# Performance work log

Hardware: AMD Instinct MI355X
Metric: run time of the kernel (lower is better)

Reference implementation:

```python
import jax, jax.numpy as jnp
import numpy as np
from jax import lax

EPS = 1e-5
DW_TH = 4.0   # threshold in cut_conv3_5_DW
PW_TH = 1e-3  # threshold in cut_conv3_5_PW


def _bn(x, gamma, beta, mean, var):
    # inference-mode batchnorm over channel dim (NCHW)
    scale = (gamma * lax.rsqrt(var + EPS))[None, :, None, None]
    shift = (beta - mean * gamma * lax.rsqrt(var + EPS))[None, :, None, None]
    return x * scale + shift


def _channel_cut(x, th):
    # faithful to max(torch.max(x[m][k]), -torch.min(x[m][k])) == max |x| per (n, c)
    max_obs = jnp.max(jnp.abs(x), axis=(2, 3), keepdims=True)  # [N, C, 1, 1]
    return jnp.where(max_obs < th, jnp.zeros_like(x), x)


def setup_inputs() -> dict:
    key = jax.random.key(0)
    ks = jax.random.split(key, 6)
    N, Cin, Cout, H, W = 32, 256, 512, 56, 56
    x = jax.random.normal(ks[0], (N, Cin, H, W), dtype=jnp.float32)
    dw_w = jax.random.normal(ks[1], (Cin, 1, 3, 3), dtype=jnp.float32) * 0.3
    dw_b = jax.random.normal(ks[2], (Cin,), dtype=jnp.float32) * 0.1
    pw_w = jax.random.normal(ks[3], (Cout, Cin), dtype=jnp.float32) * 0.05
    pw_b = jax.random.normal(ks[4], (Cout,), dtype=jnp.float32) * 0.1
    return {
        "x": x,
        "dw_w": dw_w,
        "dw_b": dw_b,
        "bn1_gamma": jnp.ones((Cin,), jnp.float32) * 2.0,
        "bn1_beta": jnp.zeros((Cin,), jnp.float32),
        "bn1_mean": jnp.zeros((Cin,), jnp.float32),
        "bn1_var": jnp.ones((Cin,), jnp.float32),
        "pw_w": pw_w,
        "pw_b": pw_b,
        "bn2_gamma": jnp.ones((Cout,), jnp.float32),
        "bn2_beta": jnp.zeros((Cout,), jnp.float32),
        "bn2_mean": jnp.zeros((Cout,), jnp.float32),
        "bn2_var": jnp.ones((Cout,), jnp.float32),
    }


def reference(x, dw_w, dw_b, bn1_gamma, bn1_beta, bn1_mean, bn1_var,
              pw_w, pw_b, bn2_gamma, bn2_beta, bn2_mean, bn2_var):
    Cin = x.shape[1]
    # depthwise 3x3 conv, padding=1 (groups == in_channels)
    y = lax.conv_general_dilated(
        x, dw_w, window_strides=(1, 1), padding=((1, 1), (1, 1)),
        dimension_numbers=("NCHW", "OIHW", "NCHW"),
        feature_group_count=Cin,
    ) + dw_b[None, :, None, None]
    y = jax.nn.relu(_bn(y, bn1_gamma, bn1_beta, bn1_mean, bn1_var))
    y = _channel_cut(y, DW_TH)
    # pointwise 1x1 conv as channel GEMM
    z = jnp.einsum("oc,nchw->nohw", pw_w, y) + pw_b[None, :, None, None]
    z = jax.nn.relu(_bn(z, bn2_gamma, bn2_beta, bn2_mean, bn2_var))
    z = _channel_cut(z, PW_TH)
    return z
```

## Files before the change

kernel.cpp:

```cpp
#include <hip/hip_runtime.h>
#include <hip/hip_bf16.h>

#define HH 56
#define WW 56
#define HW 3136
#define CIN 256
#define COUT 512
#define NBATCH 32
#define EPS 1e-5f
#define DW_TH 4.0f
#define PW_TH 1e-3f

#define CG 32
#define CPITCH 508

typedef __attribute__((ext_vector_type(8))) short s16x8;
typedef __attribute__((ext_vector_type(4))) float f32x4;
typedef unsigned int u32;
typedef unsigned short u16;

__device__ __forceinline__ void async_copy16(void* lds, const void* g) {
    __builtin_amdgcn_global_load_lds((const __attribute__((address_space(1))) unsigned int*)g,
                                     (__attribute__((address_space(3))) unsigned int*)lds,
                                     16, 0, 0);
}

__device__ __forceinline__ u16 bf16_bits(float f) {
    __hip_bfloat16 h = __float2bfloat16(f);
    union { __hip_bfloat16 h; u16 u; } cv; cv.h = h; return cv.u;
}

__global__ __launch_bounds__(256) void prep_kernel(
    const float* __restrict__ pww, const float* __restrict__ pwb,
    const float* __restrict__ g2, const float* __restrict__ b2,
    const float* __restrict__ m2, const float* __restrict__ v2,
    u16* __restrict__ wb, float2* __restrict__ scsh,
    u32* __restrict__ omax, u32* __restrict__ dwmax)
{
    const int gid = blockIdx.x * 256 + threadIdx.x;
    const int base = gid * 8;
    const float4 a = *(const float4*)(pww + base);
    const float4 b = *(const float4*)(pww + base + 4);
    union { u16 u[8]; s16x8 v; } pk;
    pk.u[0] = bf16_bits(a.x); pk.u[1] = bf16_bits(a.y);
    pk.u[2] = bf16_bits(a.z); pk.u[3] = bf16_bits(a.w);
    pk.u[4] = bf16_bits(b.x); pk.u[5] = bf16_bits(b.y);
    pk.u[6] = bf16_bits(b.z); pk.u[7] = bf16_bits(b.w);
    *(s16x8*)(wb + base) = pk.v;
    omax[gid] = 0u;
    if (gid < NBATCH * CIN) dwmax[gid] = 0u;
    if (gid < COUT) {
        const float sc = g2[gid] * rsqrtf(v2[gid] + EPS);
        const float sh = fmaf(-m2[gid], sc, b2[gid]) + pwb[gid] * sc;
        scsh[gid] = make_float2(sc, sh);
    }
}

__global__ __launch_bounds__(256) void dw_kernel(
    const float* __restrict__ x, const float* __restrict__ dww, const float* __restrict__ dwb,
    const float* __restrict__ g1, const float* __restrict__ b1,
    const float* __restrict__ m1, const float* __restrict__ v1,
    u16* __restrict__ y, u32* __restrict__ dwmax)
{
    __shared__ float xs[CG * CPITCH];

    const int bid = blockIdx.x;
    const int cg = bid & 7;
    const int hs = (bid >> 3) & 7;
    const int n  = bid >> 6;
    const int t  = threadIdx.x;

    const int g0     = hs * 7 - 1;
    const int gstart = (g0 < 0) ? 0 : g0;
    const int gend   = (hs * 7 + 7 > 55) ? 55 : hs * 7 + 7;
    const int nrows  = gend - gstart + 1;
    const int dst0   = gstart - g0;
    const int cnt4   = nrows * 14;

    if (hs == 0) {
        for (int i = t; i < CG * 14; i += 256) {
            const int c = i / 14, j = i - c * 14;
            *(float4*)&xs[c * CPITCH + j * 4] = make_float4(0.f, 0.f, 0.f, 0.f);
        }
    } else if (hs == 7) {
        for (int i = t; i < CG * 14; i += 256) {
            const int c = i / 14, j = i - c * 14;
            *(float4*)&xs[c * CPITCH + 8 * 56 + j * 4] = make_float4(0.f, 0.f, 0.f, 0.f);
        }
    }

    {
        const float* gbase = x + (size_t)(n * CIN + cg * CG) * HW + gstart * 56;
        const int half = t >> 7;
        const int i4 = t & 127;
        for (int cc = 0; cc < 16; ++cc) {
            const int c = cc * 2 + half;
            if (i4 < cnt4) {
                const float4 v = *(const float4*)(gbase + (size_t)c * HW + i4 * 4);
                *(float4*)&xs[c * CPITCH + dst0 * 56 + i4 * 4] = v;
            }
        }
    }
    __syncthreads();

    const int r = t >> 5;
    const int c = t & 31;
    float vmax = 0.f;
    if (r < 7) {
        const int ch = cg * CG + c;
        const float* wp = dww + ch * 9;
        const float w00 = wp[0], w01 = wp[1], w02 = wp[2];
        const float w10 = wp[3], w11 = wp[4], w12 = wp[5];
        const float w20 = wp[6], w21 = wp[7], w22 = wp[8];
        const float sc = g1[ch] * rsqrtf(v1[ch] + EPS);
        const float sh = fmaf(-m1[ch], sc, b1[ch]) + dwb[ch] * sc;

        const float* rm = &xs[c * CPITCH + r * 56];
        const float* r0 = rm + 56;
        const float* rp = rm + 112;
        const int grow = hs * 7 + r;
        u16* yo = y + (size_t)(n * HW + grow * WW) * CIN + ch;

        float4 cm = *(const float4*)rm;
        float4 c0 = *(const float4*)r0;
        float4 cp = *(const float4*)rp;
        float lm = 0.f, l0 = 0.f, lp = 0.f;

        for (int chk = 0; chk < 14; ++chk) {
            float4 nm, n0, np;
            if (chk < 13) {
                nm = *(const float4*)(rm + 4 * chk + 4);
                n0 = *(const float4*)(r0 + 4 * chk + 4);
                np = *(const float4*)(rp + 4 * chk + 4);
            } else {
                nm = n0 = np = make_float4(0.f, 0.f, 0.f, 0.f);
            }
            float s0 = w00*lm   + w01*cm.x + w02*cm.y
                     + w10*l0   + w11*c0.x + w12*c0.y
                     + w20*lp   + w21*cp.x + w22*cp.y;
            float s1 = w00*cm.x + w01*cm.y + w02*cm.z
                     + w10*c0.x + w11*c0.y + w12*c0.z
                     + w20*cp.x + w21*cp.y + w22*cp.z;
            float s2 = w00*cm.y + w01*cm.z + w02*cm.w
                     + w10*c0.y + w11*c0.z + w12*c0.w
                     + w20*cp.y + w21*cp.z + w22*cp.w;
            float s3 = w00*cm.z + w01*cm.w + w02*nm.x
                     + w10*c0.z + w11*c0.w + w12*n0.x
                     + w20*cp.z + w21*cp.w + w22*np.x;
            const float v0 = fmaxf(fmaf(s0, sc, sh), 0.f);
            const float v1s = fmaxf(fmaf(s1, sc, sh), 0.f);
            const float v2s = fmaxf(fmaf(s2, sc, sh), 0.f);
            const float v3 = fmaxf(fmaf(s3, sc, sh), 0.f);
            vmax = fmaxf(fmaxf(vmax, fmaxf(v0, v1s)), fmaxf(v2s, v3));
            yo[(4 * chk + 0) * CIN] = bf16_bits(v0);
            yo[(4 * chk + 1) * CIN] = bf16_bits(v1s);
            yo[(4 * chk + 2) * CIN] = bf16_bits(v2s);
            yo[(4 * chk + 3) * CIN] = bf16_bits(v3);
            lm = cm.w; l0 = c0.w; lp = cp.w;
            cm = nm; c0 = n0; cp = np;
        }
    }
    vmax = fmaxf(vmax, __shfl_xor(vmax, 32));
    if ((t & 32) == 0)
        atomicMax(&dwmax[n * CIN + cg * CG + c], __float_as_uint(vmax));
}

__global__ __launch_bounds__(64) void dwcut_kernel(const u32* __restrict__ dwmax, u16* __restrict__ y)
{
    const int b = blockIdx.x;
    if (__uint_as_float(dwmax[b]) >= DW_TH) return;
    const int n = b >> 8, c = b & 255;
    for (int hw = threadIdx.x; hw < HW; hw += 64)
        y[(size_t)(n * HW + hw) * CIN + c] = 0;
}

__global__ __launch_bounds__(256) void pw_kernel(
    const u16* __restrict__ y, const u16* __restrict__ wb,
    const float2* __restrict__ scsh,
    float* __restrict__ out, u32* __restrict__ omax)
{
    __shared__ u16 Wt[128 * 32];
    __shared__ u16 Yt[112 * 32];

    const int hwt = blockIdx.x, ot = blockIdx.y, n = blockIdx.z;
    const int t = threadIdx.x;
    const int w = t >> 6;
    const int l = t & 63;
    const int lo = l & 15, hi = l >> 4;

    const int o_blk  = ot * 128;
    const int hw_blk = n * HW + hwt * 112;

    const u16* wg  = wb + (size_t)(o_blk + w * 32 + (l >> 2)) * CIN + (l & 3) * 8;
    const u16* yg  = y  + (size_t)(hw_blk + (l >> 2)) * CIN + (l & 3) * 8;
    char* WtB = (char*)Wt;
    char* YtB = (char*)Yt;

    f32x4 acc[2][7];
#pragma unroll
    for (int s = 0; s < 2; ++s)
#pragma unroll
        for (int j = 0; j < 7; ++j) acc[s][j] = (f32x4){0.f, 0.f, 0.f, 0.f};

    for (int k0 = 0; k0 < CIN; k0 += 32) {
        async_copy16(WtB + (w * 32 + 0) * 64, wg + k0);
        async_copy16(WtB + (w * 32 + 16) * 64, wg + k0 + (size_t)16 * CIN);
        {
            const int j0 = 2 * w;
            async_copy16(YtB + j0 * 16 * 64, yg + k0 + (size_t)(j0 * 16) * CIN);
            if (j0 + 1 < 7)
                async_copy16(YtB + (j0 + 1) * 16 * 64, yg + k0 + (size_t)((j0 + 1) * 16) * CIN);
        }
        __syncthreads();

        s16x8 af[2], bf[7];
#pragma unroll
        for (int s = 0; s < 2; ++s)
            af[s] = *(const s16x8*)(WtB + (w * 32 + s * 16 + lo) * 64 + hi * 16);
#pragma unroll
        for (int j = 0; j < 7; ++j)
            bf[j] = *(const s16x8*)(YtB + (j * 16 + lo) * 64 + hi * 16);
#pragma unroll
        for (int s = 0; s < 2; ++s)
#pragma unroll
            for (int j = 0; j < 7; ++j)
                acc[s][j] = __builtin_amdgcn_mfma_f32_16x16x32_bf16(af[s], bf[j], acc[s][j], 0, 0, 0);
        __syncthreads();
    }

#pragma unroll
    for (int s = 0; s < 2; ++s) {
#pragma unroll
        for (int r = 0; r < 4; ++r) {
            const int o = o_blk + w * 32 + s * 16 + hi * 4 + r;
            const float2 ss = scsh[o];
            float m = 0.f;
            float* op = out + (size_t)(n * COUT + o) * HW + hwt * 112 + lo;
#pragma unroll
            for (int j = 0; j < 7; ++j) {
                const float v = fmaxf(fmaf(acc[s][j][r], ss.x, ss.y), 0.f);
                op[j * 16] = v;
                m = fmaxf(m, v);
            }
            m = fmaxf(m, __shfl_xor(m, 1));
            m = fmaxf(m, __shfl_xor(m, 2));
            m = fmaxf(m, __shfl_xor(m, 4));
            m = fmaxf(m, __shfl_xor(m, 8));
            if (lo == 0) atomicMax(&omax[n * COUT + o], __float_as_uint(m));
        }
    }
}

__global__ __launch_bounds__(256) void pwcut_kernel(const u32* __restrict__ omax, float* __restrict__ out)
{
    const int b = blockIdx.x;
    if (__uint_as_float(omax[b]) >= PW_TH) return;
    float* p = out + (size_t)b * HW;
    for (int i = threadIdx.x; i < HW; i += 256) p[i] = 0.0f;
}

extern "C" void kernel_launch(void* const* d_in, const int* in_sizes, int n_in,
                              void* d_out, int out_size, void* d_ws, size_t ws_size,
                              hipStream_t stream) {
    const float* x   = (const float*)d_in[0];
    const float* dww = (const float*)d_in[1];
    const float* dwb = (const float*)d_in[2];
    const float* g1  = (const float*)d_in[3];
    const float* b1  = (const float*)d_in[4];
    const float* m1  = (const float*)d_in[5];
    const float* v1  = (const float*)d_in[6];
    const float* pww = (const float*)d_in[7];
    const float* pwb = (const float*)d_in[8];
    const float* g2  = (const float*)d_in[9];
    const float* b2  = (const float*)d_in[10];
    const float* m2  = (const float*)d_in[11];
    const float* v2  = (const float*)d_in[12];
    float* out = (float*)d_out;

    u32*    omax  = (u32*)d_ws;
    u32*    dwmax = (u32*)((char*)d_ws + (64 << 10));
    float2* scsh  = (float2*)((char*)d_ws + (96 << 10));
    u16*    wbf   = (u16*)((char*)d_ws + (128 << 10));
    u16*    y     = (u16*)((char*)d_ws + (1 << 20));

    prep_kernel<<<64, 256, 0, stream>>>(pww, pwb, g2, b2, m2, v2, wbf, scsh, omax, dwmax);
    dw_kernel<<<NBATCH * 8 * 8, 256, 0, stream>>>(x, dww, dwb, g1, b1, m1, v1, y, dwmax);
    dwcut_kernel<<<NBATCH * CIN, 64, 0, stream>>>(dwmax, y);
    dim3 gpw(HW / 112, COUT / 128, NBATCH);
    pw_kernel<<<gpw, 256, 0, stream>>>(y, wbf, scsh, out, omax);
    pwcut_kernel<<<NBATCH * COUT, 256, 0, stream>>>(omax, out);
}
```

Baseline: 432.2 us.

## Fuse depthwise channel cut into pointwise GEMM via weight masking, double-buffer tiles

Removes the separate dwcut kernel. The per-(n,c) depthwise cut is instead applied inside the pointwise GEMM by ANDing weight fragments with a per-channel mask held in LDS. The GEMM tile grows to 256 output channels with double-buffered async LDS loads and launch bounds of 256x2. Blocks are remapped via an XCD-style swizzle of a flat grid. This saves a strided scatter pass over y and overlaps loads with MFMA, at the cost of more registers and LDS per block.

Result: faster. 373.7 us (-13.5%).

```diff
diff --git a/kernel.cpp b/kernel.cpp
--- a/kernel.cpp
+++ b/kernel.cpp
@@ -165,63 +165,84 @@
         atomicMax(&dwmax[n * CIN + cg * CG + c], __float_as_uint(vmax));
 }
 
-__global__ __launch_bounds__(64) void dwcut_kernel(const u32* __restrict__ dwmax, u16* __restrict__ y)
-{
-    const int b = blockIdx.x;
-    if (__uint_as_float(dwmax[b]) >= DW_TH) return;
-    const int n = b >> 8, c = b & 255;
-    for (int hw = threadIdx.x; hw < HW; hw += 64)
-        y[(size_t)(n * HW + hw) * CIN + c] = 0;
-}
-
-__global__ __launch_bounds__(256) void pw_kernel(
+__global__ __launch_bounds__(256, 2) void pw_kernel(
     const u16* __restrict__ y, const u16* __restrict__ wb,
-    const float2* __restrict__ scsh,
+    const float2* __restrict__ scsh, const u32* __restrict__ dwmax,
     float* __restrict__ out, u32* __restrict__ omax)
 {
-    __shared__ u16 Wt[128 * 32];
-    __shared__ u16 Yt[112 * 32];
-
-    const int hwt = blockIdx.x, ot = blockIdx.y, n = blockIdx.z;
+    __shared__ __align__(16) u16 Wt[2][256 * 32];
+    __shared__ __align__(16) u16 Yt[2][112 * 32];
+    __shared__ __align__(16) u16 msk[CIN];
+
+    const int bid = blockIdx.x;
+    const int g   = (bid & 7) * 224 + (bid >> 3);
+    const int ot  = g & 1;
+    const int r2  = g >> 1;
+    const int hwt = r2 % 28;
+    const int n   = r2 / 28;
+
     const int t = threadIdx.x;
     const int w = t >> 6;
     const int l = t & 63;
     const int lo = l & 15, hi = l >> 4;
 
-    const int o_blk  = ot * 128;
+    const int o_blk  = ot * 256;
     const int hw_blk = n * HW + hwt * 112;
 
-    const u16* wg  = wb + (size_t)(o_blk + w * 32 + (l >> 2)) * CIN + (l & 3) * 8;
-    const u16* yg  = y  + (size_t)(hw_blk + (l >> 2)) * CIN + (l & 3) * 8;
-    char* WtB = (char*)Wt;
-    char* YtB = (char*)Yt;
-
-    f32x4 acc[2][7];
-#pragma unroll
-    for (int s = 0; s < 2; ++s)
+    const u16* wg = wb + (size_t)(o_blk + w * 64 + (l >> 2)) * CIN + (l & 3) * 8;
+    const u16* yg = y  + (size_t)(hw_blk + (l >> 2)) * CIN + (l & 3) * 8;
+
+    msk[t] = (__uint_as_float(dwmax[n * CIN + t]) >= DW_TH) ? (u16)0xFFFFu : (u16)0u;
+
+    f32x4 acc[4][7];
+#pragma unroll
+    for (int s = 0; s < 4; ++s)
 #pragma unroll
         for (int j = 0; j < 7; ++j) acc[s][j] = (f32x4){0.f, 0.f, 0.f, 0.f};
 
-    for (int k0 = 0; k0 < CIN; k0 += 32) {
-        async_copy16(WtB + (w * 32 + 0) * 64, wg + k0);
-        async_copy16(WtB + (w * 32 + 16) * 64, wg + k0 + (size_t)16 * CIN);
-        {
+    {
+        char* WtB = (char*)&Wt[0][0];
+        char* YtB = (char*)&Yt[0][0];
+#pragma unroll
+        for (int i = 0; i < 4; ++i)
+            async_copy16(WtB + (w * 64 + i * 16) * 64 + l * 16, wg + (size_t)(i * 16) * CIN);
+        const int j0 = 2 * w;
+        async_copy16(YtB + (j0 * 16) * 64 + l * 16, yg + (size_t)(j0 * 16) * CIN);
+        if (j0 + 1 < 7)
+            async_copy16(YtB + ((j0 + 1) * 16) * 64 + l * 16, yg + (size_t)((j0 + 1) * 16) * CIN);
+    }
+    __syncthreads();
+
+#pragma unroll 2
+    for (int tk = 0; tk < 8; ++tk) {
+        const int cur = tk & 1;
+        if (tk < 7) {
+            const int k1 = (tk + 1) * 32;
+            char* WtB = (char*)&Wt[cur ^ 1][0];
+            char* YtB = (char*)&Yt[cur ^ 1][0];
+#pragma unroll
+            for (int i = 0; i < 4; ++i)
+                async_copy16(WtB + (w * 64 + i * 16) * 64 + l * 16, wg + k1 + (size_t)(i * 16) * CIN);
             const int j0 = 2 * w;
-            async_copy16(YtB + j0 * 16 * 64, yg + k0 + (size_t)(j0 * 16) * CIN);
+            async_copy16(YtB + (j0 * 16) * 64 + l * 16, yg + k1 + (size_t)(j0 * 16) * CIN);
             if (j0 + 1 < 7)
-                async_copy16(YtB + (j0 + 1) * 16 * 64, yg + k0 + (size_t)((j0 + 1) * 16) * CIN);
-        }
-        __syncthreads();
-
-        s16x8 af[2], bf[7];
-#pragma unroll
-        for (int s = 0; s < 2; ++s)
-            af[s] = *(const s16x8*)(WtB + (w * 32 + s * 16 + lo) * 64 + hi * 16);
+                async_copy16(YtB + ((j0 + 1) * 16) * 64 + l * 16, yg + k1 + (size_t)((j0 + 1) * 16) * CIN);
+        }
+        const char* WtB = (const char*)&Wt[cur][0];
+        const char* YtB = (const char*)&Yt[cur][0];
+        const s16x8 m8 = *(const s16x8*)((const char*)msk + tk * 64 + hi * 16);
+
+        s16x8 af[4], bf[7];
+#pragma unroll
+        for (int s = 0; s < 4; ++s) {
+            af[s] = *(const s16x8*)(WtB + (w * 64 + s * 16 + lo) * 64 + hi * 16);
+            af[s] = af[s] & m8;
+        }
 #pragma unroll
         for (int j = 0; j < 7; ++j)
             bf[j] = *(const s16x8*)(YtB + (j * 16 + lo) * 64 + hi * 16);
 #pragma unroll
-        for (int s = 0; s < 2; ++s)
+        for (int s = 0; s < 4; ++s)
 #pragma unroll
             for (int j = 0; j < 7; ++j)
                 acc[s][j] = __builtin_amdgcn_mfma_f32_16x16x32_bf16(af[s], bf[j], acc[s][j], 0, 0, 0);
@@ -229,10 +250,10 @@
     }
 
 #pragma unroll
-    for (int s = 0; s < 2; ++s) {
+    for (int s = 0; s < 4; ++s) {
 #pragma unroll
         for (int r = 0; r < 4; ++r) {
-            const int o = o_blk + w * 32 + s * 16 + hi * 4 + r;
+            const int o = o_blk + w * 64 + s * 16 + hi * 4 + r;
             const float2 ss = scsh[o];
             float m = 0.f;
             float* op = out + (size_t)(n * COUT + o) * HW + hwt * 112 + lo;
@@ -285,8 +306,6 @@
 
     prep_kernel<<<64, 256, 0, stream>>>(pww, pwb, g2, b2, m2, v2, wbf, scsh, omax, dwmax);
     dw_kernel<<<NBATCH * 8 * 8, 256, 0, stream>>>(x, dww, dwb, g1, b1, m1, v1, y, dwmax);
-    dwcut_kernel<<<NBATCH * CIN, 64, 0, stream>>>(dwmax, y);
-    dim3 gpw(HW / 112, COUT / 128, NBATCH);
-    pw_kernel<<<gpw, 256, 0, stream>>>(y, wbf, scsh, out, omax);
+    pw_kernel<<<1792, 256, 0, stream>>>(y, wbf, scsh, dwmax, out, omax);
     pwcut_kernel<<<NBATCH * COUT, 256, 0, stream>>>(omax, out);
 }
```
